# Performance work log

Measured on AMD Instinct MI355X. Metric: run time of the kernel, lower is better.

## Reference

```python
import jax, jax.numpy as jnp
import numpy as np

ALPHA = 1.0
EPS = 1e-6


def setup_inputs() -> dict:
    key = jax.random.key(0)
    ks = jax.random.split(key, 6)
    B, d_lat, hidden, n_genes = 256, 32, 512, 4000
    z = jax.random.normal(ks[0], (B, d_lat), dtype=jnp.float32)
    W1 = jax.random.normal(ks[1], (d_lat, hidden), dtype=jnp.float32) / np.sqrt(d_lat)
    b1 = jnp.zeros((hidden,), dtype=jnp.float32)
    W2 = jax.random.normal(ks[2], (hidden, n_genes), dtype=jnp.float32) / np.sqrt(hidden)
    b2 = jnp.zeros((n_genes,), dtype=jnp.float32)
    log_theta = 0.5 * jax.random.normal(ks[3], (n_genes,), dtype=jnp.float32)
    return {"z": z, "W1": W1, "b1": b1, "W2": W2, "b2": b2, "log_theta": log_theta}


def _decode_mu(z_vec, W1, b1, W2, b2):
    # NB decoder mean for a single latent vector; lib_dummy == 1 so no scaling.
    h = jax.nn.relu(z_vec @ W1 + b1)            # [hidden]
    return jax.nn.softplus(h @ W2 + b2)          # [n_genes]


def reference(z, W1, b1, W2, b2, log_theta):
    d_lat = z.shape[1]
    theta = jnp.exp(log_theta)                   # [G], per-gene dispersion

    f = lambda zv: _decode_mu(zv, W1, b1, W2, b2)

    mu = jax.vmap(f)(z)                          # [B, G]
    J = jax.vmap(jax.jacfwd(f))(z)               # [B, G, d_lat]

    # weights computed under no_grad in the original
    mu_ng = jax.lax.stop_gradient(mu)
    weights = theta / (mu_ng * (mu_ng + theta) + EPS)   # [B, G]

    # Gram[b, i, j] = sum_g J[b,g,i] * w[b,g] * J[b,g,j]  (== U @ U.T with U = sqrt(w)*J^T)
    Gram = jnp.einsum('bgi,bg,bgj->bij', J, weights, J)  # [B, d_lat, d_lat]

    eye = jnp.eye(d_lat, dtype=z.dtype)
    losses = jnp.sum((Gram - ALPHA * eye) ** 2, axis=(1, 2))  # [B]
    return jnp.mean(losses)
```

## Files before the change

### kernel.cpp

```cpp
#include <hip/hip_runtime.h>

typedef __bf16 bf16x8 __attribute__((ext_vector_type(8)));
typedef float f32x4 __attribute__((ext_vector_type(4)));
typedef unsigned short u16x8 __attribute__((ext_vector_type(8)));

typedef const void __attribute__((address_space(1)))* gas_ptr;
typedef void __attribute__((address_space(3)))* las_ptr;

#define GLOAD16(gp, lp) __builtin_amdgcn_global_load_lds((gas_ptr)(gp), (las_ptr)(lp), 16, 0, 0)

__device__ __forceinline__ unsigned short f2bf(float f) {
  unsigned int u = __float_as_uint(f);
  u += 0x7FFF + ((u >> 16) & 1);
  return (unsigned short)(u >> 16);
}
__device__ __forceinline__ float bf2f(unsigned short u) {
  return __uint_as_float(((unsigned int)u) << 16);
}

__global__ __launch_bounds__(256) void k_w2t(const float* __restrict__ W2,
                                             unsigned short* __restrict__ W2T) {
  __shared__ float tile[64][65];
  const int gt = blockIdx.x;
  const int jt = blockIdx.y;
  const int t = threadIdx.x;
  const int c = t & 63, r4 = t >> 6;
#pragma unroll
  for (int r = 0; r < 16; ++r) {
    int jj = r * 4 + r4;
    int g = gt * 64 + c;
    tile[jj][c] = (g < 4000) ? W2[(size_t)(jt * 64 + jj) * 4000 + g] : 0.f;
  }
  __syncthreads();
#pragma unroll
  for (int r = 0; r < 16; ++r) {
    int gg = r * 4 + r4;
    W2T[(size_t)(gt * 64 + gg) * 512 + jt * 64 + c] = f2bf(tile[c][gg]);
  }
}

__global__ __launch_bounds__(256) void k_prep(const float* __restrict__ z,
                                              const float* __restrict__ W1,
                                              const float* __restrict__ b1,
                                              unsigned short* __restrict__ Hb,
                                              unsigned short* __restrict__ Astack) {
  __shared__ float zs[32];
  __shared__ __align__(8) unsigned char mk[512];
  const int b = blockIdx.x, t = threadIdx.x;
  if (t < 32) zs[t] = z[b * 32 + t];
  __syncthreads();
#pragma unroll
  for (int jj = 0; jj < 2; ++jj) {
    int j = t + jj * 256;
    float a = b1[j];
#pragma unroll
    for (int i = 0; i < 32; ++i) a = fmaf(zs[i], W1[i * 512 + j], a);
    bool m = a > 0.f;
    mk[j] = m ? 1 : 0;
    Hb[b * 512 + j] = m ? f2bf(a) : (unsigned short)0;
  }
  __syncthreads();
#pragma unroll
  for (int k = 0; k < 8; ++k) {
    int c8 = t + k * 256;
    int row = c8 >> 6;
    int k8 = (c8 & 63) * 8;
    unsigned long long m8 = *(const unsigned long long*)(mk + k8);
    const float* w = W1 + row * 512 + k8;
    u16x8 out;
#pragma unroll
    for (int e = 0; e < 8; ++e)
      out[e] = ((m8 >> (e * 8)) & 0xffULL) ? f2bf(w[e]) : (unsigned short)0;
    *(u16x8*)(Astack + ((size_t)(b * 32 + row)) * 512 + k8) = out;
  }
}

__global__ __launch_bounds__(256) void k_s3(const unsigned short* __restrict__ Hb,
                                            const unsigned short* __restrict__ W2T,
                                            const float* __restrict__ b2,
                                            const float* __restrict__ log_theta,
                                            float* __restrict__ Cw) {
  __shared__ __align__(16) char smem[24576];
  char* Abuf = smem;
  char* Bbuf = smem + 8192;

  const int bm = blockIdx.x;
  const int g0 = blockIdx.y * 64;
  const int t = threadIdx.x;
  const int lane = t & 63;
  const int wave = t >> 6;
  const int l8 = lane >> 3;
  const int kxor = (((lane & 7) ^ l8) << 3);
  const int c16 = lane & 15;
  const int lg = lane >> 4;

  f32x4 acc[2];
  acc[0] = (f32x4){0.f, 0.f, 0.f, 0.f};
  acc[1] = (f32x4){0.f, 0.f, 0.f, 0.f};

#define STAGE_S3(buf, kt)                                                             \
  do {                                                                                \
    GLOAD16(Hb + (size_t)(bm * 32 + wave * 8 + l8) * 512 + (kt) * 64 + kxor,          \
            Abuf + (buf) * 4096 + wave * 1024);                                       \
    _Pragma("unroll") for (int qq = 0; qq < 2; ++qq) {                                \
      int q = wave * 2 + qq;                                                          \
      GLOAD16(W2T + (size_t)(g0 + q * 8 + l8) * 512 + (kt) * 64 + kxor,               \
              Bbuf + (buf) * 8192 + q * 1024);                                        \
    }                                                                                 \
  } while (0)

  STAGE_S3(0, 0);
  __syncthreads();

  for (int kt = 0; kt < 8; ++kt) {
    int cur = kt & 1;
    if (kt < 7) STAGE_S3(cur ^ 1, kt + 1);
    const char* Ab = Abuf + cur * 4096;
    const char* Bb = Bbuf + cur * 8192;
#pragma unroll
    for (int ks = 0; ks < 2; ++ks) {
      int kb = ks * 64 + lg * 16;
      bf16x8 av[2], bv;
#pragma unroll
      for (int mt = 0; mt < 2; ++mt) {
        int row = mt * 16 + c16;
        av[mt] = *(const bf16x8*)(Ab + (row >> 3) * 1024 + (row & 7) * 128 + (kb ^ ((row & 7) << 4)));
      }
      {
        int row = wave * 16 + c16;
        bv = *(const bf16x8*)(Bb + (row >> 3) * 1024 + (row & 7) * 128 + (kb ^ ((row & 7) << 4)));
      }
#pragma unroll
      for (int mt = 0; mt < 2; ++mt)
        acc[mt] = __builtin_amdgcn_mfma_f32_16x16x32_bf16(av[mt], bv, acc[mt], 0, 0, 0);
    }
    __syncthreads();
  }

  {
    int g = g0 + wave * 16 + c16;
    if (g < 4000) {
      float bb = b2[g];
      float theta = expf(log_theta[g]);
#pragma unroll
      for (int mt = 0; mt < 2; ++mt)
#pragma unroll
        for (int r = 0; r < 4; ++r) {
          int sample = bm * 32 + mt * 16 + lg * 4 + r;
          float s = acc[mt][r] + bb;
          float sig = 1.f / (1.f + expf(-s));
          float mu = (s > 20.f) ? s : log1pf(expf(s));
          float w = theta / (mu * (mu + theta) + 1e-6f);
          Cw[(size_t)sample * 4096 + g] = w * sig * sig;
        }
    } else {
#pragma unroll
      for (int mt = 0; mt < 2; ++mt)
#pragma unroll
        for (int r = 0; r < 4; ++r) {
          int sample = bm * 32 + mt * 16 + lg * 4 + r;
          Cw[(size_t)sample * 4096 + g] = 0.f;
        }
    }
  }
}

__global__ __launch_bounds__(256, 2) void k_gemm(const unsigned short* __restrict__ Astack,
                                                 const unsigned short* __restrict__ W2T,
                                                 const float* __restrict__ Cw,
                                                 float* __restrict__ Gram) {
  __shared__ __align__(16) char smem[65536];
  char* AbufB = smem;
  char* BbufB = smem + 32768;

  const int bm = blockIdx.x;
  const int g0 = blockIdx.y * 128;
  const int t = threadIdx.x;
  const int lane = t & 63;
  const int wave = t >> 6;
  const int wr = wave >> 1, wc = wave & 1;
  const int l8 = lane >> 3;
  const int kxor = (((lane & 7) ^ l8) << 3);
  const int c16 = lane & 15;
  const int lg = lane >> 4;

  f32x4 acc[4][4];
#pragma unroll
  for (int mt = 0; mt < 4; ++mt)
#pragma unroll
    for (int nt = 0; nt < 4; ++nt) acc[mt][nt] = (f32x4){0.f, 0.f, 0.f, 0.f};

  const size_t Abase = (size_t)bm * 128 * 512;

#define STAGE_G(buf, kt)                                                              \
  do {                                                                                \
    _Pragma("unroll") for (int qq = 0; qq < 4; ++qq) {                                \
      int q = wave * 4 + qq;                                                          \
      GLOAD16(Astack + Abase + (size_t)(q * 8 + l8) * 512 + (kt) * 64 + kxor,         \
              AbufB + (buf) * 16384 + q * 1024);                                      \
    }                                                                                 \
    _Pragma("unroll") for (int qq = 0; qq < 4; ++qq) {                                \
      int q = wave * 4 + qq;                                                          \
      GLOAD16(W2T + (size_t)(g0 + q * 8 + l8) * 512 + (kt) * 64 + kxor,               \
              BbufB + (buf) * 16384 + q * 1024);                                      \
    }                                                                                 \
  } while (0)

  STAGE_G(0, 0);
  __syncthreads();

  for (int kt = 0; kt < 8; ++kt) {
    int cur = kt & 1;
    if (kt < 7) STAGE_G(cur ^ 1, kt + 1);
    const char* Ab = AbufB + cur * 16384;
    const char* Bb = BbufB + cur * 16384;
#pragma unroll
    for (int ks = 0; ks < 2; ++ks) {
      int kb = ks * 64 + lg * 16;
      bf16x8 av[4], bv[4];
#pragma unroll
      for (int mt = 0; mt < 4; ++mt) {
        int row = wr * 64 + mt * 16 + c16;
        av[mt] = *(const bf16x8*)(Ab + (row >> 3) * 1024 + (row & 7) * 128 + (kb ^ ((row & 7) << 4)));
      }
#pragma unroll
      for (int nt = 0; nt < 4; ++nt) {
        int row = wc * 64 + nt * 16 + c16;
        bv[nt] = *(const bf16x8*)(Bb + (row >> 3) * 1024 + (row & 7) * 128 + (kb ^ ((row & 7) << 4)));
      }
#pragma unroll
      for (int mt = 0; mt < 4; ++mt)
#pragma unroll
        for (int nt = 0; nt < 4; ++nt)
          acc[mt][nt] = __builtin_amdgcn_mfma_f32_16x16x32_bf16(av[mt], bv[nt], acc[mt][nt], 0, 0, 0);
    }
    __syncthreads();
  }

  unsigned short* T = (unsigned short*)smem;
  float* c_lds = (float*)(smem + 34816);

#pragma unroll
  for (int mt = 0; mt < 4; ++mt)
#pragma unroll
    for (int nt = 0; nt < 4; ++nt)
#pragma unroll
      for (int r = 0; r < 4; ++r) {
        int row = wr * 64 + mt * 16 + lg * 4 + r;
        int col = wc * 64 + nt * 16 + c16;
        T[row * 136 + col] = f2bf(acc[mt][nt][r]);
      }
#pragma unroll
  for (int k = 0; k < 2; ++k) {
    int e = t + k * 256;
    c_lds[e] = Cw[(size_t)(bm * 4 + (e >> 7)) * 4096 + g0 + (e & 127)];
  }
  __syncthreads();

  {
    const int s = wave;
    f32x4 gacc[2][2];
#pragma unroll
    for (int m2 = 0; m2 < 2; ++m2)
#pragma unroll
      for (int n2 = 0; n2 < 2; ++n2) gacc[m2][n2] = (f32x4){0.f, 0.f, 0.f, 0.f};

#pragma unroll
    for (int ch = 0; ch < 4; ++ch) {
      u16x8 raw[2];
      bf16x8 ap[2], bp[2];
      f32x4 cv0 = *(const f32x4*)(c_lds + s * 128 + ch * 32 + lg * 8);
      f32x4 cv1 = *(const f32x4*)(c_lds + s * 128 + ch * 32 + lg * 8 + 4);
#pragma unroll
      for (int m2 = 0; m2 < 2; ++m2) {
        int row = s * 32 + m2 * 16 + c16;
        raw[m2] = *(const u16x8*)((const char*)T + row * 272 + ch * 64 + lg * 16);
        u16x8 sc;
#pragma unroll
        for (int e = 0; e < 4; ++e) sc[e] = f2bf(bf2f(raw[m2][e]) * cv0[e]);
#pragma unroll
        for (int e = 0; e < 4; ++e) sc[4 + e] = f2bf(bf2f(raw[m2][4 + e]) * cv1[e]);
        ap[m2] = __builtin_bit_cast(bf16x8, sc);
        bp[m2] = __builtin_bit_cast(bf16x8, raw[m2]);
      }
#pragma unroll
      for (int m2 = 0; m2 < 2; ++m2)
#pragma unroll
        for (int n2 = 0; n2 < 2; ++n2)
          gacc[m2][n2] = __builtin_amdgcn_mfma_f32_16x16x32_bf16(ap[m2], bp[n2], gacc[m2][n2], 0, 0, 0);
    }

#pragma unroll
    for (int m2 = 0; m2 < 2; ++m2)
#pragma unroll
      for (int n2 = 0; n2 < 2; ++n2)
#pragma unroll
        for (int r = 0; r < 4; ++r) {
          int i = m2 * 16 + lg * 4 + r;
          int j = n2 * 16 + c16;
          atomicAdd(Gram + (size_t)(bm * 4 + s) * 1024 + i * 32 + j, gacc[m2][n2][r]);
        }
  }
}

__global__ __launch_bounds__(256) void k_loss(const float* __restrict__ Gram,
                                              float* __restrict__ out) {
  __shared__ float red[4];
  const int b = blockIdx.x, t = threadIdx.x;
  float local = 0.f;
#pragma unroll
  for (int k = 0; k < 4; ++k) {
    int e = t + k * 256;
    float d = Gram[(size_t)b * 1024 + e] - (((e >> 5) == (e & 31)) ? 1.f : 0.f);
    local += d * d;
  }
#pragma unroll
  for (int off = 32; off > 0; off >>= 1) local += __shfl_down(local, off);
  if ((t & 63) == 0) red[t >> 6] = local;
  __syncthreads();
  if (t == 0) {
    float s = red[0] + red[1] + red[2] + red[3];
    atomicAdd(out, s * (1.f / 256.f));
  }
}

extern "C" void kernel_launch(void* const* d_in, const int* in_sizes, int n_in,
                              void* d_out, int out_size, void* d_ws, size_t ws_size,
                              hipStream_t stream) {
  const float* z = (const float*)d_in[0];
  const float* W1 = (const float*)d_in[1];
  const float* b1 = (const float*)d_in[2];
  const float* W2 = (const float*)d_in[3];
  const float* b2 = (const float*)d_in[4];
  const float* lt = (const float*)d_in[5];

  char* ws = (char*)d_ws;
  unsigned short* W2T = (unsigned short*)ws;
  unsigned short* Astack = (unsigned short*)(ws + 4194304);
  unsigned short* Hb = (unsigned short*)(ws + 12582912);
  float* Cw = (float*)(ws + 12976128);
  float* Gram = (float*)(ws + 17170432);

  hipMemsetAsync(Gram, 0, 256 * 1024 * 4, stream);
  hipMemsetAsync(d_out, 0, 4, stream);

  k_w2t<<<dim3(64, 8), 256, 0, stream>>>(W2, W2T);
  k_prep<<<256, 256, 0, stream>>>(z, W1, b1, Hb, Astack);
  k_s3<<<dim3(8, 64), 256, 0, stream>>>(Hb, W2T, b2, lt, Cw);
  k_gemm<<<dim3(64, 32), 256, 0, stream>>>(Astack, W2T, Cw, Gram);
  k_loss<<<256, 256, 0, stream>>>(Gram, (float*)d_out);
}
```

Before: 152.9 us.

## Enlarge GEMM tiles to 256x256 with 512 threads and merge prep kernels

The Gram GEMM now uses 256x256 output tiles with 8 waves and 136KB of dynamic LDS, so each block covers 8 samples and 256 genes and loads of A and B are reused across more outputs. It also uses an XOR-swizzled staging layout for the transposed tile. The W2 transpose and the W1/ReLU prep kernels are fused into one launch so that one kernel launch disappears. The cost is much lower occupancy: 512 blocks need 136KB of LDS each, which likely allows one block per CU, and the register pressure per thread is higher.

```diff
diff --git a/kernel.cpp b/kernel.cpp
--- a/kernel.cpp
+++ b/kernel.cpp
@@ -18,60 +18,64 @@
   return __uint_as_float(((unsigned int)u) << 16);
 }
 
-__global__ __launch_bounds__(256) void k_w2t(const float* __restrict__ W2,
-                                             unsigned short* __restrict__ W2T) {
+__global__ __launch_bounds__(256) void k_prep2(const float* __restrict__ W2,
+                                               unsigned short* __restrict__ W2T,
+                                               const float* __restrict__ z,
+                                               const float* __restrict__ W1,
+                                               const float* __restrict__ b1,
+                                               unsigned short* __restrict__ Hb,
+                                               unsigned short* __restrict__ Astack) {
   __shared__ float tile[64][65];
-  const int gt = blockIdx.x;
-  const int jt = blockIdx.y;
   const int t = threadIdx.x;
-  const int c = t & 63, r4 = t >> 6;
-#pragma unroll
-  for (int r = 0; r < 16; ++r) {
-    int jj = r * 4 + r4;
-    int g = gt * 64 + c;
-    tile[jj][c] = (g < 4000) ? W2[(size_t)(jt * 64 + jj) * 4000 + g] : 0.f;
-  }
-  __syncthreads();
-#pragma unroll
-  for (int r = 0; r < 16; ++r) {
-    int gg = r * 4 + r4;
-    W2T[(size_t)(gt * 64 + gg) * 512 + jt * 64 + c] = f2bf(tile[c][gg]);
-  }
-}
-
-__global__ __launch_bounds__(256) void k_prep(const float* __restrict__ z,
-                                              const float* __restrict__ W1,
-                                              const float* __restrict__ b1,
-                                              unsigned short* __restrict__ Hb,
-                                              unsigned short* __restrict__ Astack) {
-  __shared__ float zs[32];
-  __shared__ __align__(8) unsigned char mk[512];
-  const int b = blockIdx.x, t = threadIdx.x;
-  if (t < 32) zs[t] = z[b * 32 + t];
-  __syncthreads();
-#pragma unroll
-  for (int jj = 0; jj < 2; ++jj) {
-    int j = t + jj * 256;
-    float a = b1[j];
-#pragma unroll
-    for (int i = 0; i < 32; ++i) a = fmaf(zs[i], W1[i * 512 + j], a);
-    bool m = a > 0.f;
-    mk[j] = m ? 1 : 0;
-    Hb[b * 512 + j] = m ? f2bf(a) : (unsigned short)0;
-  }
-  __syncthreads();
-#pragma unroll
-  for (int k = 0; k < 8; ++k) {
-    int c8 = t + k * 256;
-    int row = c8 >> 6;
-    int k8 = (c8 & 63) * 8;
-    unsigned long long m8 = *(const unsigned long long*)(mk + k8);
-    const float* w = W1 + row * 512 + k8;
-    u16x8 out;
-#pragma unroll
-    for (int e = 0; e < 8; ++e)
-      out[e] = ((m8 >> (e * 8)) & 0xffULL) ? f2bf(w[e]) : (unsigned short)0;
-    *(u16x8*)(Astack + ((size_t)(b * 32 + row)) * 512 + k8) = out;
+  if (blockIdx.y < 8) {
+    const int gt = blockIdx.x;
+    const int jt = blockIdx.y;
+    const int c = t & 63, r4 = t >> 6;
+#pragma unroll
+    for (int r = 0; r < 16; ++r) {
+      int jj = r * 4 + r4;
+      int g = gt * 64 + c;
+      tile[jj][c] = (g < 4000) ? W2[(size_t)(jt * 64 + jj) * 4000 + g] : 0.f;
+    }
+    __syncthreads();
+#pragma unroll
+    for (int r = 0; r < 16; ++r) {
+      int gg = r * 4 + r4;
+      W2T[(size_t)(gt * 64 + gg) * 512 + jt * 64 + c] = f2bf(tile[c][gg]);
+    }
+  } else {
+    float* zs = &tile[0][0];
+    unsigned char* mk = (unsigned char*)&tile[2][0];
+    for (int s = 0; s < 4; ++s) {
+      int b = blockIdx.x * 4 + s;
+      __syncthreads();
+      if (t < 32) zs[t] = z[b * 32 + t];
+      __syncthreads();
+#pragma unroll
+      for (int jj = 0; jj < 2; ++jj) {
+        int j = t + jj * 256;
+        float a = b1[j];
+#pragma unroll
+        for (int i = 0; i < 32; ++i) a = fmaf(zs[i], W1[i * 512 + j], a);
+        bool m = a > 0.f;
+        mk[j] = m ? 1 : 0;
+        Hb[b * 512 + j] = m ? f2bf(a) : (unsigned short)0;
+      }
+      __syncthreads();
+#pragma unroll
+      for (int k = 0; k < 8; ++k) {
+        int c8 = t + k * 256;
+        int row = c8 >> 6;
+        int k8 = (c8 & 63) * 8;
+        unsigned long long m8 = *(const unsigned long long*)(mk + k8);
+        const float* w = W1 + row * 512 + k8;
+        u16x8 out;
+#pragma unroll
+        for (int e = 0; e < 8; ++e)
+          out[e] = ((m8 >> (e * 8)) & 0xffULL) ? f2bf(w[e]) : (unsigned short)0;
+        *(u16x8*)(Astack + ((size_t)(b * 32 + row)) * 512 + k8) = out;
+      }
+    }
   }
 }
 
@@ -165,71 +169,69 @@
   }
 }
 
-__global__ __launch_bounds__(256, 2) void k_gemm(const unsigned short* __restrict__ Astack,
+__global__ __launch_bounds__(512, 2) void k_gemm(const unsigned short* __restrict__ Astack,
                                                  const unsigned short* __restrict__ W2T,
                                                  const float* __restrict__ Cw,
                                                  float* __restrict__ Gram) {
-  __shared__ __align__(16) char smem[65536];
+  extern __shared__ __align__(16) char smem[];
   char* AbufB = smem;
-  char* BbufB = smem + 32768;
+  char* BbufB = smem + 65536;
 
   const int bm = blockIdx.x;
-  const int g0 = blockIdx.y * 128;
+  const int g0 = blockIdx.y * 256;
   const int t = threadIdx.x;
   const int lane = t & 63;
   const int wave = t >> 6;
-  const int wr = wave >> 1, wc = wave & 1;
-  const int l8 = lane >> 3;
-  const int kxor = (((lane & 7) ^ l8) << 3);
+  const int wr = wave >> 2;
+  const int wc = wave & 3;
+  const int kxor = (((t & 7) ^ ((t >> 3) & 7)) << 3);
   const int c16 = lane & 15;
   const int lg = lane >> 4;
 
-  f32x4 acc[4][4];
-#pragma unroll
-  for (int mt = 0; mt < 4; ++mt)
+  f32x4 acc[8][4];
+#pragma unroll
+  for (int mt = 0; mt < 8; ++mt)
 #pragma unroll
     for (int nt = 0; nt < 4; ++nt) acc[mt][nt] = (f32x4){0.f, 0.f, 0.f, 0.f};
 
-  const size_t Abase = (size_t)bm * 128 * 512;
-
-#define STAGE_G(buf, kt)                                                              \
+  const unsigned short* Aptr = Astack + (size_t)bm * 256 * 512;
+  const unsigned short* Bptr = W2T + (size_t)g0 * 512;
+  const int trow = t >> 3;
+
+#define STAGE_BIG(buf, kt)                                                            \
   do {                                                                                \
-    _Pragma("unroll") for (int qq = 0; qq < 4; ++qq) {                                \
-      int q = wave * 4 + qq;                                                          \
-      GLOAD16(Astack + Abase + (size_t)(q * 8 + l8) * 512 + (kt) * 64 + kxor,         \
-              AbufB + (buf) * 16384 + q * 1024);                                      \
-    }                                                                                 \
-    _Pragma("unroll") for (int qq = 0; qq < 4; ++qq) {                                \
-      int q = wave * 4 + qq;                                                          \
-      GLOAD16(W2T + (size_t)(g0 + q * 8 + l8) * 512 + (kt) * 64 + kxor,               \
-              BbufB + (buf) * 16384 + q * 1024);                                      \
-    }                                                                                 \
+    _Pragma("unroll") for (int q = 0; q < 4; ++q)                                     \
+      GLOAD16(Aptr + (size_t)(q * 64 + trow) * 512 + (kt) * 64 + kxor,                \
+              AbufB + (buf) * 32768 + q * 8192 + wave * 1024);                        \
+    _Pragma("unroll") for (int q = 0; q < 4; ++q)                                     \
+      GLOAD16(Bptr + (size_t)(q * 64 + trow) * 512 + (kt) * 64 + kxor,                \
+              BbufB + (buf) * 32768 + q * 8192 + wave * 1024);                        \
   } while (0)
 
-  STAGE_G(0, 0);
+  STAGE_BIG(0, 0);
   __syncthreads();
 
   for (int kt = 0; kt < 8; ++kt) {
     int cur = kt & 1;
-    if (kt < 7) STAGE_G(cur ^ 1, kt + 1);
-    const char* Ab = AbufB + cur * 16384;
-    const char* Bb = BbufB + cur * 16384;
+    if (kt < 7) STAGE_BIG(cur ^ 1, kt + 1);
+    const char* Ab = AbufB + cur * 32768;
+    const char* Bb = BbufB + cur * 32768;
 #pragma unroll
     for (int ks = 0; ks < 2; ++ks) {
       int kb = ks * 64 + lg * 16;
-      bf16x8 av[4], bv[4];
-#pragma unroll
-      for (int mt = 0; mt < 4; ++mt) {
-        int row = wr * 64 + mt * 16 + c16;
-        av[mt] = *(const bf16x8*)(Ab + (row >> 3) * 1024 + (row & 7) * 128 + (kb ^ ((row & 7) << 4)));
+      bf16x8 av[8], bv[4];
+#pragma unroll
+      for (int mt = 0; mt < 8; ++mt) {
+        int row = wr * 128 + mt * 16 + c16;
+        av[mt] = *(const bf16x8*)(Ab + row * 128 + (kb ^ ((row & 7) << 4)));
       }
 #pragma unroll
       for (int nt = 0; nt < 4; ++nt) {
         int row = wc * 64 + nt * 16 + c16;
-        bv[nt] = *(const bf16x8*)(Bb + (row >> 3) * 1024 + (row & 7) * 128 + (kb ^ ((row & 7) << 4)));
-      }
-#pragma unroll
-      for (int mt = 0; mt < 4; ++mt)
+        bv[nt] = *(const bf16x8*)(Bb + row * 128 + (kb ^ ((row & 7) << 4)));
+      }
+#pragma unroll
+      for (int mt = 0; mt < 8; ++mt)
 #pragma unroll
         for (int nt = 0; nt < 4; ++nt)
           acc[mt][nt] = __builtin_amdgcn_mfma_f32_16x16x32_bf16(av[mt], bv[nt], acc[mt][nt], 0, 0, 0);
@@ -237,23 +239,22 @@
     __syncthreads();
   }
 
-  unsigned short* T = (unsigned short*)smem;
-  float* c_lds = (float*)(smem + 34816);
-
-#pragma unroll
-  for (int mt = 0; mt < 4; ++mt)
+  float* c_lds = (float*)(smem + 131072);
+
+#pragma unroll
+  for (int mt = 0; mt < 8; ++mt)
 #pragma unroll
     for (int nt = 0; nt < 4; ++nt)
 #pragma unroll
       for (int r = 0; r < 4; ++r) {
-        int row = wr * 64 + mt * 16 + lg * 4 + r;
+        int row = wr * 128 + mt * 16 + lg * 4 + r;
         int col = wc * 64 + nt * 16 + c16;
-        T[row * 136 + col] = f2bf(acc[mt][nt][r]);
-      }
-#pragma unroll
-  for (int k = 0; k < 2; ++k) {
-    int e = t + k * 256;
-    c_lds[e] = Cw[(size_t)(bm * 4 + (e >> 7)) * 4096 + g0 + (e & 127)];
+        *(unsigned short*)(smem + row * 512 + ((col * 2) ^ ((row & 7) << 4))) = f2bf(acc[mt][nt][r]);
+      }
+#pragma unroll
+  for (int k = 0; k < 4; ++k) {
+    int e = t + k * 512;
+    c_lds[e] = Cw[(size_t)(bm * 8 + (e >> 8)) * 4096 + g0 + (e & 255)];
   }
   __syncthreads();
 
@@ -266,15 +267,15 @@
       for (int n2 = 0; n2 < 2; ++n2) gacc[m2][n2] = (f32x4){0.f, 0.f, 0.f, 0.f};
 
 #pragma unroll
-    for (int ch = 0; ch < 4; ++ch) {
+    for (int ch = 0; ch < 8; ++ch) {
+      f32x4 cv0 = *(const f32x4*)(c_lds + s * 256 + ch * 32 + lg * 8);
+      f32x4 cv1 = *(const f32x4*)(c_lds + s * 256 + ch * 32 + lg * 8 + 4);
       u16x8 raw[2];
       bf16x8 ap[2], bp[2];
-      f32x4 cv0 = *(const f32x4*)(c_lds + s * 128 + ch * 32 + lg * 8);
-      f32x4 cv1 = *(const f32x4*)(c_lds + s * 128 + ch * 32 + lg * 8 + 4);
 #pragma unroll
       for (int m2 = 0; m2 < 2; ++m2) {
         int row = s * 32 + m2 * 16 + c16;
-        raw[m2] = *(const u16x8*)((const char*)T + row * 272 + ch * 64 + lg * 16);
+        raw[m2] = *(const u16x8*)(smem + row * 512 + ((ch * 64 + lg * 16) ^ ((row & 7) << 4)));
         u16x8 sc;
 #pragma unroll
         for (int e = 0; e < 4; ++e) sc[e] = f2bf(bf2f(raw[m2][e]) * cv0[e]);
@@ -298,7 +299,7 @@
         for (int r = 0; r < 4; ++r) {
           int i = m2 * 16 + lg * 4 + r;
           int j = n2 * 16 + c16;
-          atomicAdd(Gram + (size_t)(bm * 4 + s) * 1024 + i * 32 + j, gacc[m2][n2][r]);
+          atomicAdd(Gram + (size_t)(bm * 8 + s) * 1024 + i * 32 + j, gacc[m2][n2][r]);
         }
   }
 }
@@ -344,9 +345,11 @@
   hipMemsetAsync(Gram, 0, 256 * 1024 * 4, stream);
   hipMemsetAsync(d_out, 0, 4, stream);
 
-  k_w2t<<<dim3(64, 8), 256, 0, stream>>>(W2, W2T);
-  k_prep<<<256, 256, 0, stream>>>(z, W1, b1, Hb, Astack);
+  static const int kGemmLds = 131072 + 8192;
+  hipFuncSetAttribute((const void*)k_gemm, hipFuncAttributeMaxDynamicSharedMemorySize, kGemmLds);
+
+  k_prep2<<<dim3(64, 9), 256, 0, stream>>>(W2, W2T, z, W1, b1, Hb, Astack);
   k_s3<<<dim3(8, 64), 256, 0, stream>>>(Hb, W2T, b2, lt, Cw);
-  k_gemm<<<dim3(64, 32), 256, 0, stream>>>(Astack, W2T, Cw, Gram);
+  k_gemm<<<dim3(32, 16), 512, kGemmLds, stream>>>(Astack, W2T, Cw, Gram);
   k_loss<<<256, 256, 0, stream>>>(Gram, (float*)d_out);
 }
```

Result: slower. 166.8 us (+9.1%).
